# Kernel optimization log

Measured on AMD Instinct MI355X. Metric: run time of the kernel, lower is better.

## Reference

```python
import jax, jax.numpy as jnp
import numpy as np

D_IN, D_K, D_V = 768, 128, 768


def setup_inputs() -> dict:
    key = jax.random.key(0)
    ks = jax.random.split(key, 7)
    x = jax.random.normal(ks[0], (4, 2048, D_IN), dtype=jnp.float32)
    s_in = 1.0 / np.sqrt(D_IN)
    Wq = jax.random.uniform(ks[1], (D_IN, D_K), minval=-s_in, maxval=s_in, dtype=jnp.float32)
    bq = jax.random.uniform(ks[2], (D_K,), minval=-s_in, maxval=s_in, dtype=jnp.float32)
    Wk = jax.random.uniform(ks[3], (D_IN, D_K), minval=-s_in, maxval=s_in, dtype=jnp.float32)
    bk = jax.random.uniform(ks[4], (D_K,), minval=-s_in, maxval=s_in, dtype=jnp.float32)
    Wv = jax.random.uniform(ks[5], (D_IN, D_V), minval=-s_in, maxval=s_in, dtype=jnp.float32)
    bv = jax.random.uniform(ks[6], (D_V,), minval=-s_in, maxval=s_in, dtype=jnp.float32)
    return {"x": x, "Wq": Wq, "bq": bq, "Wk": Wk, "bk": bk, "Wv": Wv, "bv": bv}


def reference(x, Wq, bq, Wk, bk, Wv, bv):
    # q,k: [b,t,d_k]; v: [b,t,d_v]
    q = jnp.einsum('bti,ik->btk', x, Wq) + bq
    k = jnp.einsum('bti,ik->btk', x, Wk) + bk
    v = jnp.einsum('bti,iv->btv', x, Wv) + bv
    scale = 1.0 / jnp.sqrt(jnp.asarray(D_K, dtype=jnp.float32))
    scores = jnp.einsum('bqk,btk->bqt', q, k) * scale  # [b,t,t]
    attn = jax.nn.softmax(scores, axis=-1)
    return jnp.einsum('bqt,btv->bqv', attn, v)
```

## Files before the change

kernel.cpp:

```cpp
#include <hip/hip_runtime.h>
#include <stdint.h>

typedef unsigned short u16;
typedef __attribute__((ext_vector_type(8))) short short8;
typedef __attribute__((ext_vector_type(4))) float f32x4;

#define BATCH 4
#define SEQ   2048
#define DIN   768
#define DK    128
#define DV    768
#define MTOT  (BATCH*SEQ)
#define NQKV  1024

__device__ __forceinline__ u16 f2bf(float f) {
  union { float f; uint32_t u; } v; v.f = f;
  uint32_t r = v.u + 0x7FFFu + ((v.u >> 16) & 1u);
  return (u16)(r >> 16);
}
__device__ __forceinline__ float bf2f(u16 h) {
  union { uint32_t u; float f; } v; v.u = ((uint32_t)h) << 16;
  return v.f;
}

__global__ void pack_weights(const float* __restrict__ Wq, const float* __restrict__ bq,
                             const float* __restrict__ Wk, const float* __restrict__ bk,
                             const float* __restrict__ Wv, const float* __restrict__ bv,
                             u16* __restrict__ WbT, float* __restrict__ biasP) {
  const float qs = 0.088388347648318447f;
  int n = blockIdx.x;
  if (threadIdx.x == 0) {
    float b = (n < DK) ? bq[n] * qs : (n < 2*DK ? bk[n - DK] : bv[n - 2*DK]);
    biasP[n] = b;
  }
  const float* col; int cn, ldw; float sc;
  if (n < DK)        { col = Wq; cn = n;        ldw = DK; sc = qs;   }
  else if (n < 2*DK) { col = Wk; cn = n - DK;   ldw = DK; sc = 1.0f; }
  else               { col = Wv; cn = n - 2*DK; ldw = DV; sc = 1.0f; }
  for (int i = threadIdx.x; i < DIN; i += blockDim.x) {
    WbT[(size_t)n * DIN + i] = f2bf(col[(size_t)i * ldw + cn] * sc);
  }
}

__global__ void convert_x(const float* __restrict__ x, u16* __restrict__ xb) {
  int i = (blockIdx.x * blockDim.x + threadIdx.x) * 4;
  float4 v = *(const float4*)(x + i);
  u16 o[4] = { f2bf(v.x), f2bf(v.y), f2bf(v.z), f2bf(v.w) };
  *(uint2*)(xb + i) = *(const uint2*)o;
}

template<bool OUT_BF16, bool HAS_BIAS>
__global__ __launch_bounds__(512, 4) void gemm_nt(
    const u16* __restrict__ A, int lda, long long sA,
    const u16* __restrict__ BT, int ldb, long long sB,
    void* __restrict__ Cv, int ldc, long long sC,
    int K, int gx, int gy, const float* __restrict__ bias)
{
  __shared__ u16 As[2][128][64];
  __shared__ u16 Bs[2][128][64];
  const int tid = threadIdx.x;
  const int l   = tid & 63;
  const int wid = tid >> 6;
  const int wm  = wid >> 2;
  const int wn  = wid & 3;

  const int nwg = gridDim.x;
  const int cpx = nwg >> 3;
  const int bid = blockIdx.x;
  const int wg  = (bid & 7) * cpx + (bid >> 3);
  const int z   = wg / (gx * gy);
  const int rem = wg - z * gx * gy;
  const int by  = rem / gx;
  const int bx  = rem - by * gx;
  const int m0  = bx * 128;
  const int n0  = by * 128;

  A  += (size_t)z * (size_t)sA;
  BT += (size_t)z * (size_t)sB;

  f32x4 acc[4][2] = {};

  const int lr = l >> 3;
  const int lc = ((l & 7) ^ lr) * 8;

  const int ca = wid * 4;
  auto STAGE = [&](int buf, int k0) {
#pragma unroll
    for (int i = 0; i < 4; ++i) {
      int c = ca + i;
      if (c < 16) {
        const u16* src = A + (size_t)(m0 + c * 8 + lr) * lda + k0 + lc;
        __builtin_amdgcn_global_load_lds(
            (const __attribute__((address_space(1))) unsigned int*)src,
            (__attribute__((address_space(3))) unsigned int*)&As[buf][c * 8][0],
            16, 0, 0);
      } else {
        int cb = c - 16;
        const u16* src = BT + (size_t)(n0 + cb * 8 + lr) * ldb + k0 + lc;
        __builtin_amdgcn_global_load_lds(
            (const __attribute__((address_space(1))) unsigned int*)src,
            (__attribute__((address_space(3))) unsigned int*)&Bs[buf][cb * 8][0],
            16, 0, 0);
      }
    }
  };

  STAGE(0, 0);
  __syncthreads();

  int cur = 0;
  for (int k0 = 0; k0 < K; k0 += 64) {
    if (k0 + 64 < K) STAGE(cur ^ 1, k0 + 64);
#pragma unroll
    for (int ks = 0; ks < 2; ++ks) {
      short8 af[4], bg[2];
#pragma unroll
      for (int i = 0; i < 4; ++i) {
        int row  = wm * 64 + i * 16 + (l & 15);
        int slot = (ks * 4 + (l >> 4)) ^ (row & 7);
        af[i] = *(const short8*)&As[cur][row][slot * 8];
      }
#pragma unroll
      for (int j = 0; j < 2; ++j) {
        int row  = wn * 32 + j * 16 + (l & 15);
        int slot = (ks * 4 + (l >> 4)) ^ (row & 7);
        bg[j] = *(const short8*)&Bs[cur][row][slot * 8];
      }
#pragma unroll
      for (int i = 0; i < 4; ++i)
#pragma unroll
        for (int j = 0; j < 2; ++j)
          acc[i][j] = __builtin_amdgcn_mfma_f32_16x16x32_bf16(af[i], bg[j], acc[i][j], 0, 0, 0);
    }
    __syncthreads();
    cur ^= 1;
  }

  const int rbase = (l >> 4) * 4;
  const int cl    = l & 15;
#pragma unroll
  for (int i = 0; i < 4; ++i) {
#pragma unroll
    for (int j = 0; j < 2; ++j) {
      int col = n0 + wn * 32 + j * 16 + cl;
      float bv_ = HAS_BIAS ? bias[col] : 0.0f;
#pragma unroll
      for (int q = 0; q < 4; ++q) {
        int row = m0 + wm * 64 + i * 16 + rbase + q;
        float v = acc[i][j][q] + bv_;
        if (OUT_BF16)
          ((u16*)Cv)[(size_t)z * (size_t)sC + (size_t)row * ldc + col] = f2bf(v);
        else
          ((float*)Cv)[(size_t)z * (size_t)sC + (size_t)row * ldc + col] = v;
      }
    }
  }
}

__global__ void transpose_v(const u16* __restrict__ qkv, u16* __restrict__ vT) {
  __shared__ u16 tile[64][72];
  int b  = blockIdx.z;
  int t0 = blockIdx.x * 64;
  int j0 = blockIdx.y * 64;
  int tid = threadIdx.x;
  int tr = tid >> 2;
  int tc = (tid & 3) * 16;
  const u16* src = qkv + (size_t)(b * SEQ + t0 + tr) * NQKV + 2 * DK + j0 + tc;
  uint4 v0 = *(const uint4*)src;
  uint4 v1 = *(const uint4*)(src + 8);
  *(uint4*)&tile[tr][tc]     = v0;
  *(uint4*)&tile[tr][tc + 8] = v1;
  __syncthreads();
  u16 tmp[16];
#pragma unroll
  for (int u = 0; u < 16; ++u) tmp[u] = tile[tc + u][tr];
  u16* dst = vT + ((size_t)b * DV + j0 + tr) * SEQ + t0 + tc;
  *(uint4*)dst       = *(const uint4*)&tmp[0];
  *(uint4*)(dst + 8) = *(const uint4*)&tmp[8];
}

__global__ __launch_bounds__(256) void softmax_rows(u16* __restrict__ S) {
  int row = blockIdx.x * 4 + (threadIdx.x >> 6);
  int l   = threadIdx.x & 63;
  u16* p = S + (size_t)row * SEQ;
  uint4 d[4];
#pragma unroll
  for (int c = 0; c < 4; ++c) d[c] = *(const uint4*)(p + l * 8 + c * 512);
  float v[32];
  float mx = -1e30f;
#pragma unroll
  for (int c = 0; c < 4; ++c) {
    const u16* u = (const u16*)&d[c];
#pragma unroll
    for (int e = 0; e < 8; ++e) { float f = bf2f(u[e]); v[c * 8 + e] = f; mx = fmaxf(mx, f); }
  }
#pragma unroll
  for (int s = 32; s; s >>= 1) mx = fmaxf(mx, __shfl_xor(mx, s, 64));
  float sum = 0.0f;
#pragma unroll
  for (int e = 0; e < 32; ++e) { float ex = __expf(v[e] - mx); v[e] = ex; sum += ex; }
#pragma unroll
  for (int s = 32; s; s >>= 1) sum += __shfl_xor(sum, s, 64);
  float inv = 1.0f / sum;
#pragma unroll
  for (int c = 0; c < 4; ++c) {
    u16 o[8];
#pragma unroll
    for (int e = 0; e < 8; ++e) o[e] = f2bf(v[c * 8 + e] * inv);
    *(uint4*)(p + l * 8 + c * 512) = *(const uint4*)o;
  }
}

extern "C" void kernel_launch(void* const* d_in, const int* in_sizes, int n_in,
                              void* d_out, int out_size, void* d_ws, size_t ws_size,
                              hipStream_t stream) {
  const float* x  = (const float*)d_in[0];
  const float* Wq = (const float*)d_in[1];
  const float* bq = (const float*)d_in[2];
  const float* Wk = (const float*)d_in[3];
  const float* bk = (const float*)d_in[4];
  const float* Wv = (const float*)d_in[5];
  const float* bv = (const float*)d_in[6];
  float* out = (float*)d_out;

  size_t off = 0;
  auto alloc = [&](size_t bytes) -> void* {
    void* p = (char*)d_ws + off;
    off += (bytes + 255) & ~(size_t)255;
    return p;
  };
  u16*   xb    = (u16*)alloc((size_t)MTOT * DIN * 2);
  u16*   WbT   = (u16*)alloc((size_t)NQKV * DIN * 2);
  float* biasP = (float*)alloc(NQKV * 4);
  u16*   qkv   = (u16*)alloc((size_t)MTOT * NQKV * 2);
  u16*   vT    = (u16*)alloc((size_t)BATCH * DV * SEQ * 2);
  u16*   S     = (u16*)alloc((size_t)BATCH * SEQ * SEQ * 2);
  if (off > ws_size) return;

  pack_weights<<<dim3(NQKV), dim3(256), 0, stream>>>(Wq, bq, Wk, bk, Wv, bv, WbT, biasP);
  convert_x<<<dim3((MTOT * DIN / 4) / 256), dim3(256), 0, stream>>>(x, xb);

  gemm_nt<true, true><<<dim3(64 * 8), dim3(512), 0, stream>>>(
      xb, DIN, 0, WbT, DIN, 0, qkv, NQKV, 0, DIN, 64, 8, biasP);

  transpose_v<<<dim3(SEQ / 64, DV / 64, BATCH), dim3(256), 0, stream>>>(qkv, vT);

  gemm_nt<true, false><<<dim3(16 * 16 * BATCH), dim3(512), 0, stream>>>(
      qkv, NQKV, (long long)SEQ * NQKV,
      qkv + DK, NQKV, (long long)SEQ * NQKV,
      S, SEQ, (long long)SEQ * SEQ, DK, 16, 16, nullptr);

  softmax_rows<<<dim3(MTOT / 4), dim3(256), 0, stream>>>(S);

  gemm_nt<false, false><<<dim3(16 * 6 * BATCH), dim3(512), 0, stream>>>(
      S, SEQ, (long long)SEQ * SEQ,
      vT, SEQ, (long long)DV * SEQ,
      out, DV, (long long)SEQ * DV, SEQ, 16, 6, nullptr);
}
```

Before: 103.0 us.

## Fuse V transpose into QKV GEMM epilogue and widen PV GEMM tile

The QKV projection epilogue now writes Q/K into a compact 256-wide buffer and writes V directly in transposed layout, which removes the separate transpose_v kernel and its round trip through global memory. The GEMM is templated on its N tile width, and the final attention-times-V GEMM uses a 128x192 tile (NJ=3), giving fewer workgroups (256 instead of 384) with more work each. Risks are uncoalesced 8-byte transposed stores in the epilogue, higher register and LDS pressure with NJ=3, and lower occupancy from the smaller grid.

```diff
diff --git a/kernel.cpp b/kernel.cpp
--- a/kernel.cpp
+++ b/kernel.cpp
@@ -49,15 +49,15 @@
   *(uint2*)(xb + i) = *(const uint2*)o;
 }
 
-template<bool OUT_BF16, bool HAS_BIAS>
+template<int MODE, int NJ>
 __global__ __launch_bounds__(512, 4) void gemm_nt(
     const u16* __restrict__ A, int lda, long long sA,
     const u16* __restrict__ BT, int ldb, long long sB,
-    void* __restrict__ Cv, int ldc, long long sC,
+    void* __restrict__ C0, void* __restrict__ C1, int ldc, long long sC,
     int K, int gx, int gy, const float* __restrict__ bias)
 {
   __shared__ u16 As[2][128][64];
-  __shared__ u16 Bs[2][128][64];
+  __shared__ u16 Bs[2][NJ * 64][64];
   const int tid = threadIdx.x;
   const int l   = tid & 63;
   const int wid = tid >> 6;
@@ -73,20 +73,21 @@
   const int by  = rem / gx;
   const int bx  = rem - by * gx;
   const int m0  = bx * 128;
-  const int n0  = by * 128;
+  const int n0  = by * (NJ * 64);
 
   A  += (size_t)z * (size_t)sA;
   BT += (size_t)z * (size_t)sB;
 
-  f32x4 acc[4][2] = {};
+  f32x4 acc[4][NJ] = {};
 
   const int lr = l >> 3;
   const int lc = ((l & 7) ^ lr) * 8;
 
-  const int ca = wid * 4;
+  const int CH = 2 + NJ;
+  const int ca = wid * CH;
   auto STAGE = [&](int buf, int k0) {
 #pragma unroll
-    for (int i = 0; i < 4; ++i) {
+    for (int i = 0; i < CH; ++i) {
       int c = ca + i;
       if (c < 16) {
         const u16* src = A + (size_t)(m0 + c * 8 + lr) * lda + k0 + lc;
@@ -113,7 +114,7 @@
     if (k0 + 64 < K) STAGE(cur ^ 1, k0 + 64);
 #pragma unroll
     for (int ks = 0; ks < 2; ++ks) {
-      short8 af[4], bg[2];
+      short8 af[4], bg[NJ];
 #pragma unroll
       for (int i = 0; i < 4; ++i) {
         int row  = wm * 64 + i * 16 + (l & 15);
@@ -121,15 +122,15 @@
         af[i] = *(const short8*)&As[cur][row][slot * 8];
       }
 #pragma unroll
-      for (int j = 0; j < 2; ++j) {
-        int row  = wn * 32 + j * 16 + (l & 15);
+      for (int j = 0; j < NJ; ++j) {
+        int row  = wn * (NJ * 16) + j * 16 + (l & 15);
         int slot = (ks * 4 + (l >> 4)) ^ (row & 7);
         bg[j] = *(const short8*)&Bs[cur][row][slot * 8];
       }
 #pragma unroll
       for (int i = 0; i < 4; ++i)
 #pragma unroll
-        for (int j = 0; j < 2; ++j)
+        for (int j = 0; j < NJ; ++j)
           acc[i][j] = __builtin_amdgcn_mfma_f32_16x16x32_bf16(af[i], bg[j], acc[i][j], 0, 0, 0);
     }
     __syncthreads();
@@ -141,42 +142,33 @@
 #pragma unroll
   for (int i = 0; i < 4; ++i) {
 #pragma unroll
-    for (int j = 0; j < 2; ++j) {
-      int col = n0 + wn * 32 + j * 16 + cl;
-      float bv_ = HAS_BIAS ? bias[col] : 0.0f;
-#pragma unroll
-      for (int q = 0; q < 4; ++q) {
-        int row = m0 + wm * 64 + i * 16 + rbase + q;
-        float v = acc[i][j][q] + bv_;
-        if (OUT_BF16)
-          ((u16*)Cv)[(size_t)z * (size_t)sC + (size_t)row * ldc + col] = f2bf(v);
-        else
-          ((float*)Cv)[(size_t)z * (size_t)sC + (size_t)row * ldc + col] = v;
+    for (int j = 0; j < NJ; ++j) {
+      int col = n0 + wn * (NJ * 16) + j * 16 + cl;
+      int row0 = m0 + wm * 64 + i * 16 + rbase;
+      if (MODE == 0) {
+#pragma unroll
+        for (int q = 0; q < 4; ++q)
+          ((float*)C0)[(size_t)z * (size_t)sC + (size_t)(row0 + q) * ldc + col] = acc[i][j][q];
+      } else if (MODE == 1) {
+#pragma unroll
+        for (int q = 0; q < 4; ++q)
+          ((u16*)C0)[(size_t)z * (size_t)sC + (size_t)(row0 + q) * ldc + col] = f2bf(acc[i][j][q]);
+      } else {
+        float bv_ = bias[col];
+        if (n0 < 256) {
+#pragma unroll
+          for (int q = 0; q < 4; ++q)
+            ((u16*)C0)[(size_t)(row0 + q) * 256 + col] = f2bf(acc[i][j][q] + bv_);
+        } else {
+          int b = row0 >> 11, t = row0 & 2047;
+          u16 o[4];
+#pragma unroll
+          for (int q = 0; q < 4; ++q) o[q] = f2bf(acc[i][j][q] + bv_);
+          *(uint2*)&((u16*)C1)[((size_t)b * DV + (col - 256)) * SEQ + t] = *(const uint2*)o;
+        }
       }
     }
   }
-}
-
-__global__ void transpose_v(const u16* __restrict__ qkv, u16* __restrict__ vT) {
-  __shared__ u16 tile[64][72];
-  int b  = blockIdx.z;
-  int t0 = blockIdx.x * 64;
-  int j0 = blockIdx.y * 64;
-  int tid = threadIdx.x;
-  int tr = tid >> 2;
-  int tc = (tid & 3) * 16;
-  const u16* src = qkv + (size_t)(b * SEQ + t0 + tr) * NQKV + 2 * DK + j0 + tc;
-  uint4 v0 = *(const uint4*)src;
-  uint4 v1 = *(const uint4*)(src + 8);
-  *(uint4*)&tile[tr][tc]     = v0;
-  *(uint4*)&tile[tr][tc + 8] = v1;
-  __syncthreads();
-  u16 tmp[16];
-#pragma unroll
-  for (int u = 0; u < 16; ++u) tmp[u] = tile[tc + u][tr];
-  u16* dst = vT + ((size_t)b * DV + j0 + tr) * SEQ + t0 + tc;
-  *(uint4*)dst       = *(const uint4*)&tmp[0];
-  *(uint4*)(dst + 8) = *(const uint4*)&tmp[8];
 }
 
 __global__ __launch_bounds__(256) void softmax_rows(u16* __restrict__ S) {
@@ -232,7 +224,7 @@
   u16*   xb    = (u16*)alloc((size_t)MTOT * DIN * 2);
   u16*   WbT   = (u16*)alloc((size_t)NQKV * DIN * 2);
   float* biasP = (float*)alloc(NQKV * 4);
-  u16*   qkv   = (u16*)alloc((size_t)MTOT * NQKV * 2);
+  u16*   qk    = (u16*)alloc((size_t)MTOT * 256 * 2);
   u16*   vT    = (u16*)alloc((size_t)BATCH * DV * SEQ * 2);
   u16*   S     = (u16*)alloc((size_t)BATCH * SEQ * SEQ * 2);
   if (off > ws_size) return;
@@ -240,20 +232,18 @@
   pack_weights<<<dim3(NQKV), dim3(256), 0, stream>>>(Wq, bq, Wk, bk, Wv, bv, WbT, biasP);
   convert_x<<<dim3((MTOT * DIN / 4) / 256), dim3(256), 0, stream>>>(x, xb);
 
-  gemm_nt<true, true><<<dim3(64 * 8), dim3(512), 0, stream>>>(
-      xb, DIN, 0, WbT, DIN, 0, qkv, NQKV, 0, DIN, 64, 8, biasP);
-
-  transpose_v<<<dim3(SEQ / 64, DV / 64, BATCH), dim3(256), 0, stream>>>(qkv, vT);
-
-  gemm_nt<true, false><<<dim3(16 * 16 * BATCH), dim3(512), 0, stream>>>(
-      qkv, NQKV, (long long)SEQ * NQKV,
-      qkv + DK, NQKV, (long long)SEQ * NQKV,
-      S, SEQ, (long long)SEQ * SEQ, DK, 16, 16, nullptr);
+  gemm_nt<2, 2><<<dim3(64 * 8), dim3(512), 0, stream>>>(
+      xb, DIN, 0, WbT, DIN, 0, qk, vT, 0, 0, DIN, 64, 8, biasP);
+
+  gemm_nt<1, 2><<<dim3(16 * 16 * BATCH), dim3(512), 0, stream>>>(
+      qk, 256, (long long)SEQ * 256,
+      qk + DK, 256, (long long)SEQ * 256,
+      S, nullptr, SEQ, (long long)SEQ * SEQ, DK, 16, 16, nullptr);
 
   softmax_rows<<<dim3(MTOT / 4), dim3(256), 0, stream>>>(S);
 
-  gemm_nt<false, false><<<dim3(16 * 6 * BATCH), dim3(512), 0, stream>>>(
+  gemm_nt<0, 3><<<dim3(16 * 4 * BATCH), dim3(512), 0, stream>>>(
       S, SEQ, (long long)SEQ * SEQ,
       vT, SEQ, (long long)DV * SEQ,
-      out, DV, (long long)SEQ * DV, SEQ, 16, 6, nullptr);
-}
+      out, nullptr, DV, (long long)SEQ * DV, SEQ, 16, 4, nullptr);
+}
```

Result: faster. 99.14 us (-3.7%).
